# Performance work log

Measured on AMD Instinct MI355X. Metric: run time of the kernel, lower is better.

Reference implementation:

```python
import jax, jax.numpy as jnp
import numpy as np

N_NODES = 16384
N_EDGES = 65536
B = 256
L = 1000
BN_EPS = 1e-5


def _bn_last(h, g, b, m, v):
    # BatchNorm1d in eval mode over last (feature) axis
    return (h - m) / jnp.sqrt(v + BN_EPS) * g + b


def _bn_chan(h, g, b, m, v):
    # BatchNorm1d in eval mode over channel axis of [N, C, W]
    inv = g / jnp.sqrt(v + BN_EPS)
    return (h - m[None, :, None]) * inv[None, :, None] + b[None, :, None]


def _conv1d(x, W, b):
    # x: [N, C, W], W: [O, I, K], stride 1, VALID
    y = jax.lax.conv_general_dilated(x, W, (1,), 'VALID',
                                     dimension_numbers=('NCH', 'OIH', 'NCH'))
    return y + b[None, :, None]


def _forward(x, g1_W1, g1_b1, g1_W2, g1_b2, gW1, gb1, gW2, gb2,
             bn_gamma, bn_beta, bn_mean, bn_var, fcxd_W, fcxd_b, embed,
             c1_W, c1_b, c2_W, c2_b, c3_W, c3_b,
             cbn_gamma, cbn_beta, cbn_mean, cbn_var, fcxc_W, fcxc_b,
             bnfc_gamma, bnfc_beta, bnfc_mean, bnfc_var,
             fc1_W, fc1_b, fc2_W, fc2_b, out_W, out_b,
             edge_index, batch, target):
    src, dst = edge_index[0], edge_index[1]
    # GIN layer 1: out_i = MLP(x_i + sum_{j->i} x_j)  (eps = 0)
    agg = jax.ops.segment_sum(x[src], dst, num_segments=N_NODES)
    h = x + agg
    h = jnp.maximum(h @ g1_W1 + g1_b1, 0.0) @ g1_W2 + g1_b2
    h = _bn_last(jnp.maximum(h, 0.0), bn_gamma[0], bn_beta[0], bn_mean[0], bn_var[0])
    # GIN layers 2..5 (stacked params)
    for i in range(4):
        agg = jax.ops.segment_sum(h[src], dst, num_segments=N_NODES)
        t = h + agg
        t = jnp.maximum(t @ gW1[i] + gb1[i], 0.0) @ gW2[i] + gb2[i]
        h = _bn_last(jnp.maximum(t, 0.0), bn_gamma[i + 1], bn_beta[i + 1],
                     bn_mean[i + 1], bn_var[i + 1])
    # global_add_pool over graph ids
    pooled = jax.ops.segment_sum(h, batch, num_segments=B)          # [B, 32]
    xd = jnp.maximum(pooled @ fcxd_W + fcxd_b, 0.0)                 # [B, 128] (dropout: eval)
    # protein branch
    emb = embed[target]                                             # [B, L, 128]
    xd2 = jnp.broadcast_to(xd[:, None, :], (B, L, xd.shape[-1]))
    xc = jnp.concatenate([emb, xd2], axis=-1).transpose(0, 2, 1)    # [B, 256, L]
    conv_params = [(c1_W, c1_b), (c2_W, c2_b), (c3_W, c3_b)]
    for i in range(3):
        xc = _conv1d(xc, conv_params[i][0], conv_params[i][1])
        xc = jnp.maximum(_bn_chan(xc, cbn_gamma[i], cbn_beta[i],
                                  cbn_mean[i], cbn_var[i]), 0.0)
    xcm = jnp.max(xc, axis=-1)                                      # global max pool -> [B, 32]
    xcf = jnp.maximum(_bn_last(xcm @ fcxc_W + fcxc_b,
                               bnfc_gamma, bnfc_beta, bnfc_mean, bnfc_var), 0.0)
    z = jnp.concatenate([xd, xcf], axis=1)                          # [B, 256]
    z = jnp.maximum(z @ fc1_W + fc1_b, 0.0)
    z = jnp.maximum(z @ fc2_W + fc2_b, 0.0)
    return z @ out_W + out_b                                        # [B, 1]


def setup_inputs() -> dict:
    key = jax.random.key(0)
    ks = list(jax.random.split(key, 48))
    it = iter(range(48))
    f32 = jnp.float32

    def rn(sh, s=0.1):
        return jax.random.normal(ks[next(it)], sh, dtype=f32) * s

    def un(sh):
        return jax.random.uniform(ks[next(it)], sh, dtype=f32, minval=0.5, maxval=1.5)

    inp = {}
    inp['x'] = jax.random.normal(ks[next(it)], (N_NODES, 78), dtype=f32)
    inp['edge_index'] = jax.random.randint(ks[next(it)], (2, N_EDGES), 0, N_NODES, dtype=jnp.int32)
    inp['batch'] = jnp.sort(jax.random.randint(ks[next(it)], (N_NODES,), 0, B, dtype=jnp.int32))
    inp['target'] = jax.random.randint(ks[next(it)], (B, L), 0, 26, dtype=jnp.int32)
    inp['g1_W1'] = rn((78, 32)); inp['g1_b1'] = rn((32,))
    inp['g1_W2'] = rn((32, 32)); inp['g1_b2'] = rn((32,))
    inp['gW1'] = rn((4, 32, 32)); inp['gb1'] = rn((4, 32))
    inp['gW2'] = rn((4, 32, 32)); inp['gb2'] = rn((4, 32))
    inp['bn_gamma'] = un((5, 32)); inp['bn_beta'] = rn((5, 32))
    inp['bn_mean'] = rn((5, 32)); inp['bn_var'] = un((5, 32))
    inp['fcxd_W'] = rn((32, 128)); inp['fcxd_b'] = rn((128,))
    inp['embed'] = rn((26, 128), 1.0)
    inp['c1_W'] = rn((32, 256, 16)); inp['c1_b'] = rn((32,))
    inp['c2_W'] = rn((32, 32, 16)); inp['c2_b'] = rn((32,))
    inp['c3_W'] = rn((32, 32, 16)); inp['c3_b'] = rn((32,))
    inp['cbn_gamma'] = un((3, 32)); inp['cbn_beta'] = rn((3, 32))
    inp['cbn_mean'] = rn((3, 32)); inp['cbn_var'] = un((3, 32))
    inp['fcxc_W'] = rn((32, 128)); inp['fcxc_b'] = rn((128,))
    inp['bnfc_gamma'] = un((128,)); inp['bnfc_beta'] = rn((128,))
    inp['bnfc_mean'] = rn((128,)); inp['bnfc_var'] = un((128,))
    inp['fc1_W'] = rn((256, 1024)); inp['fc1_b'] = rn((1024,))
    inp['fc2_W'] = rn((1024, 256)); inp['fc2_b'] = rn((256,))
    inp['out_W'] = rn((256, 1)); inp['out_b'] = rn((1,))
    return inp


def reference(x, edge_index, batch, target, g1_W1, g1_b1, g1_W2, g1_b2,
              gW1, gb1, gW2, gb2, bn_gamma, bn_beta, bn_mean, bn_var,
              fcxd_W, fcxd_b, embed, c1_W, c1_b, c2_W, c2_b, c3_W, c3_b,
              cbn_gamma, cbn_beta, cbn_mean, cbn_var, fcxc_W, fcxc_b,
              bnfc_gamma, bnfc_beta, bnfc_mean, bnfc_var,
              fc1_W, fc1_b, fc2_W, fc2_b, out_W, out_b):
    return _forward(x, g1_W1, g1_b1, g1_W2, g1_b2, gW1, gb1, gW2, gb2,
                    bn_gamma, bn_beta, bn_mean, bn_var, fcxd_W, fcxd_b, embed,
                    c1_W, c1_b, c2_W, c2_b, c3_W, c3_b,
                    cbn_gamma, cbn_beta, cbn_mean, cbn_var, fcxc_W, fcxc_b,
                    bnfc_gamma, bnfc_beta, bnfc_mean, bnfc_var,
                    fc1_W, fc1_b, fc2_W, fc2_b, out_W, out_b,
                    edge_index, batch, target)
```

## Files before the change

### kernel.cpp

```cpp
#include <hip/hip_runtime.h>
#include <hip/hip_bf16.h>

typedef __hip_bfloat16 bf16;
__device__ __forceinline__ float b2f(bf16 v){ return __bfloat162float(v); }

typedef __attribute__((ext_vector_type(8))) short s8v;
typedef __attribute__((ext_vector_type(4))) float f4v;

#define N_NODES 16384
#define N_EDGES 65536
#define NB 256
#define LSEQ 1000
#define BN_EPS 1e-5f
#define W1O 985
#define W2O 970
#define W3O 955
#define C1S 988
#define C2S 976

__device__ int g_isf32;

__device__ __forceinline__ float LD(const void* p, int i, int f){
    return f ? ((const float*)p)[i] : b2f(((const bf16*)p)[i]);
}

__device__ __forceinline__ unsigned short f2b(float x){
    unsigned u = __float_as_uint(x);
    return (unsigned short)((u + 0x7FFFu + ((u >> 16) & 1u)) >> 16);
}
__device__ __forceinline__ float bb2f(unsigned short h){
    return __uint_as_float(((unsigned)h) << 16);
}

__global__ void k_dtype(const void* x){
    if (threadIdx.x != 0 || blockIdx.x != 0) return;
    const unsigned short* u = (const unsigned short*)x;
    int insane = 0;
    for (int i = 0; i < 512; i++){
        unsigned short h = u[i];
        int ex = (h >> 7) & 0xFF;
        if (!(h == 0 || (ex >= 96 && ex <= 142))) insane++;
    }
    g_isf32 = (insane > 50) ? 1 : 0;
}

__device__ float g_hA[N_NODES*32];
__device__ float g_hB[N_NODES*32];
__device__ float g_pooled[NB*32];
__device__ float g_xd[NB*128];
__device__ float g_P[16*26*32];
__device__ float g_wsum[32*128];
__device__ float g_xdb[NB*32];
__device__ float g_xcm[NB*32];
__device__ float g_xcf[NB*128];
__device__ float g_z1[NB*1024];
__device__ float g_z2[NB*256];
__device__ float g_c1o[NB*32*C1S];
__device__ float g_c2o[NB*32*C2S];
__device__ __attribute__((aligned(16))) unsigned short g_wf[2][32768];
__device__ int g_deg[N_NODES];
__device__ int g_cur[N_NODES];
__device__ int g_rowptr[N_NODES + 1];
__device__ int g_csrc[N_EDGES];
__device__ int g_gstart[NB + 1];

__global__ void k_zero(){
    int i = blockIdx.x*256 + threadIdx.x;
    if (i < N_NODES) g_deg[i] = 0;
    else g_xcm[i - N_NODES] = 0.f;
}

__global__ void k_count(const int* __restrict__ ei){
    int e = blockIdx.x*256 + threadIdx.x;
    atomicAdd(&g_deg[ei[N_EDGES + e]], 1);
}
__global__ __launch_bounds__(1024) void k_scan(){
    __shared__ int part[1024];
    int t = threadIdx.x;
    int base = t*16;
    int s = 0;
    #pragma unroll
    for (int i = 0; i < 16; i++) s += g_deg[base + i];
    part[t] = s;
    __syncthreads();
    for (int off = 1; off < 1024; off <<= 1){
        int v = (t >= off) ? part[t - off] : 0;
        __syncthreads();
        part[t] += v;
        __syncthreads();
    }
    int run = (t == 0) ? 0 : part[t - 1];
    for (int i = 0; i < 16; i++){
        g_rowptr[base + i] = run;
        g_cur[base + i] = run;
        run += g_deg[base + i];
    }
    if (t == 1023) g_rowptr[N_NODES] = run;
}
__global__ void k_fill(const int* __restrict__ ei){
    int e = blockIdx.x*256 + threadIdx.x;
    int d = ei[N_EDGES + e];
    int slot = atomicAdd(&g_cur[d], 1);
    g_csrc[slot] = ei[e];
}
__global__ void k_ranges(const int* __restrict__ batch){
    int b = threadIdx.x;
    int lo = 0, hi = N_NODES;
    while (lo < hi){ int mid = (lo + hi) >> 1; if (batch[mid] < b) lo = mid + 1; else hi = mid; }
    g_gstart[b] = lo;
    if (b == 0) g_gstart[NB] = N_NODES;
}

__global__ void k_wpack(const void* w2, const void* w3){
    const int F = g_isf32;
    int idx = blockIdx.x*256 + threadIdx.x;
    int sel = idx >> 15;
    int r = idx & 32767;
    int j = r & 7;
    int lane = (r >> 3) & 63;
    int hl = (r >> 9) & 1;
    int ogrp = (r >> 10) & 1;
    int ktg = r >> 11;
    int c = (lane >> 4)*8 + j;
    int o = ogrp*16 + (lane & 15);
    const void* Wt = sel ? w3 : w2;
    float wv = LD(Wt, o*512 + c*16 + ktg, F);
    unsigned short h = f2b(wv);
    g_wf[sel][r] = hl ? f2b(wv - bb2f(h)) : h;
}


__global__ __launch_bounds__(256) void k_proj78(const void* x, const void* W1)
{
    const int F = g_isf32;
    __shared__ float sW1[78*32];
    __shared__ float sx[8][78];
    int tid = threadIdx.x;
    for (int i = tid; i < 78*32; i += 256) sW1[i] = LD(W1, i, F);
    int nodeBase = blockIdx.x * 8;
    for (int i = tid; i < 8*78; i += 256){
        int ln = i / 78, f = i - ln*78;
        sx[ln][f] = LD(x, (nodeBase + ln)*78 + f, F);
    }
    __syncthreads();
    int ln = tid >> 5, j = tid & 31;
    float a = 0.f;
    #pragma unroll 6
    for (int i = 0; i < 78; i++) a += sx[ln][i] * sW1[i*32 + j];
    g_hA[(nodeBase + ln)*32 + j] = a;
}

__global__ __launch_bounds__(256) void k_gin1b(
    const void* b1, const void* W2, const void* b2,
    const void* bng, const void* bnb, const void* bnm, const void* bnv)
{
    const int F = g_isf32;
    __shared__ float sW2[32*32];
    __shared__ float sb1[32], sb2[32], sA[32], sB[32];
    __shared__ float st[8][32];
    int tid = threadIdx.x;
    for (int i = tid; i < 1024; i += 256) sW2[i] = LD(W2, i, F);
    if (tid < 32){
        sb1[tid] = LD(b1, tid, F); sb2[tid] = LD(b2, tid, F);
        float inv = LD(bng, tid, F) * rsqrtf(LD(bnv, tid, F) + BN_EPS);
        sA[tid] = inv;
        sB[tid] = LD(bnb, tid, F) - LD(bnm, tid, F) * inv;
    }
    __syncthreads();
    int ln = tid >> 5, j = tid & 31;
    int n = blockIdx.x*8 + ln;
    int rs = g_rowptr[n], re2 = g_rowptr[n + 1];
    float agg = 0.f;
    for (int e = rs; e < re2; e++) agg += g_hA[g_csrc[e]*32 + j];
    st[ln][j] = fmaxf(g_hA[n*32 + j] + agg + sb1[j], 0.f);
    __syncthreads();
    float t2 = sb2[j];
    #pragma unroll
    for (int i = 0; i < 32; i++) t2 += st[ln][i] * sW2[i*32 + j];
    t2 = fmaxf(t2, 0.f);
    g_hB[n*32 + j] = t2 * sA[j] + sB[j];
}

__global__ __launch_bounds__(256) void k_gin32L(
    const void* W1, const void* b1, const void* W2, const void* b2,
    const void* bng, const void* bnb, const void* bnm, const void* bnv, int l)
{
    const int F = g_isf32;
    const float* hin = (l & 1) ? g_hA : g_hB;
    float* hout = (l & 1) ? g_hB : g_hA;
    const int oW = l*1024, ob = l*32, obn = (l+1)*32;
    __shared__ float sW1[32*32], sW2[32*32];
    __shared__ float sb1[32], sb2[32], sA[32], sB[32];
    __shared__ float sh[8][32], st[8][32];
    int tid = threadIdx.x;
    for (int i = tid; i < 1024; i += 256){ sW1[i] = LD(W1, oW + i, F); sW2[i] = LD(W2, oW + i, F); }
    if (tid < 32){
        sb1[tid] = LD(b1, ob + tid, F); sb2[tid] = LD(b2, ob + tid, F);
        float inv = LD(bng, obn + tid, F) * rsqrtf(LD(bnv, obn + tid, F) + BN_EPS);
        sA[tid] = inv;
        sB[tid] = LD(bnb, obn + tid, F) - LD(bnm, obn + tid, F) * inv;
    }
    int ln = tid >> 5, j = tid & 31;
    int n = blockIdx.x*8 + ln;
    int rs = g_rowptr[n], re2 = g_rowptr[n + 1];
    float agg = 0.f;
    for (int e = rs; e < re2; e++) agg += hin[g_csrc[e]*32 + j];
    sh[ln][j] = hin[n*32 + j] + agg;
    __syncthreads();
    float t1 = sb1[j];
    #pragma unroll
    for (int i = 0; i < 32; i++) t1 += sh[ln][i] * sW1[i*32 + j];
    st[ln][j] = fmaxf(t1, 0.f);
    __syncthreads();
    float t2 = sb2[j];
    #pragma unroll
    for (int i = 0; i < 32; i++) t2 += st[ln][i] * sW2[i*32 + j];
    t2 = fmaxf(t2, 0.f);
    hout[n*32 + j] = t2 * sA[j] + sB[j];
}

__global__ __launch_bounds__(256) void k_pool(){
    __shared__ float red[8][32];
    int b = blockIdx.x, tid = threadIdx.x;
    int j = tid & 31, sub = tid >> 5;
    int s = g_gstart[b], e = g_gstart[b + 1];
    float a = 0.f;
    for (int n = s + sub; n < e; n += 8) a += g_hB[n*32 + j];
    red[sub][j] = a;
    __syncthreads();
    if (sub == 0){
        float r = red[0][j] + red[1][j] + red[2][j] + red[3][j]
                + red[4][j] + red[5][j] + red[6][j] + red[7][j];
        g_pooled[b*32 + j] = r;
    }
}

__global__ void k_xd(const void* W, const void* bias){
    const int F = g_isf32;
    __shared__ float sp[32];
    int b = blockIdx.x, j = threadIdx.x;
    if (j < 32) sp[j] = g_pooled[b*32 + j];
    __syncthreads();
    float a = LD(bias, j, F);
    #pragma unroll
    for (int i = 0; i < 32; i++) a += sp[i] * LD(W, i*128 + j, F);
    g_xd[b*128 + j] = fmaxf(a, 0.f);
}


__global__ void k_P(const void* embed, const void* c1W){
    const int F = g_isf32;
    int idx = blockIdx.x*256 + threadIdx.x;
    if (idx >= 16*26*32) return;
    int o = idx & 31;
    int t = (idx >> 5) % 26;
    int k = idx / (32*26);
    float a = 0.f;
    for (int c = 0; c < 128; c++)
        a += LD(embed, t*128 + c, F) * LD(c1W, o*4096 + c*16 + k, F);
    g_P[(k*26 + t)*32 + o] = a;
}

__global__ void k_wsum(const void* c1W){
    const int F = g_isf32;
    int idx = blockIdx.x*256 + threadIdx.x;
    int o = idx >> 7, c = idx & 127;
    float a = 0.f;
    #pragma unroll
    for (int k = 0; k < 16; k++) a += LD(c1W, o*4096 + (128 + c)*16 + k, F);
    g_wsum[o*128 + c] = a;
}

__global__ void k_xdbias(const void* c1b){
    const int F = g_isf32;
    int idx = blockIdx.x*256 + threadIdx.x;
    int b = idx >> 5, o = idx & 31;
    float a = LD(c1b, o, F);
    for (int c = 0; c < 128; c++) a += g_xd[b*128 + c] * g_wsum[o*128 + c];
    g_xdb[idx] = a;
}

__global__ __launch_bounds__(256) void k_conv1L(
    const int* __restrict__ target,
    const void* g, const void* be, const void* m, const void* v, int obn)
{
    const int F = g_isf32;
    __shared__ float sP[16*26*32];
    __shared__ int   stg[LSEQ];
    __shared__ float sxb[32], sA[32], sB[32];
    int b = blockIdx.x, tid = threadIdx.x;
    for (int i = tid; i < 16*26*32; i += 256) sP[i] = g_P[i];
    for (int i = tid; i < LSEQ; i += 256) stg[i] = target[b*LSEQ + i];
    if (tid < 32){
        sxb[tid] = g_xdb[b*32 + tid];
        float inv = LD(g, obn + tid, F) * rsqrtf(LD(v, obn + tid, F) + BN_EPS);
        sA[tid] = inv;
        sB[tid] = LD(be, obn + tid, F) - LD(m, obn + tid, F) * inv;
    }
    __syncthreads();
    int o = tid & 31, wsub = tid >> 5;
    float xb = sxb[o], aa = sA[o], bb = sB[o];
    for (int w = wsub; w < W1O; w += 8){
        float a = xb;
        #pragma unroll
        for (int k = 0; k < 16; k++)
            a += sP[(k*26 + stg[w + k])*32 + o];
        g_c1o[(b*32 + o)*C1S + w] = fmaxf(a * aa + bb, 0.f);
    }
}


#define CT_W 128
#define CT_R 144
#define CPAD 40

__global__ __launch_bounds__(256) void k_cmfma(
    int sel, int Wvalid, int Wout, int inStride,
    const void* bias, const void* g, const void* be,
    const void* m, const void* v, int obn)
{
    const int F = g_isf32;
    const float* in = (sel == 0) ? g_c1o : g_c2o;
    __shared__ __attribute__((aligned(16))) unsigned short sAh[CT_R*CPAD];
    __shared__ __attribute__((aligned(16))) unsigned short sAl[CT_R*CPAD];
    __shared__ float sSc[32], sOf[32];
    int tid = threadIdx.x;
    int b = blockIdx.x >> 3;
    int tile = blockIdx.x & 7;
    int wbase = tile * CT_W;

    for (int c = 0; c < 32; c++){
        const float* src = in + (b*32 + c)*inStride;
        if (tid < CT_R){
            int wg_ = wbase + tid;
            float xv = (wg_ < Wvalid) ? src[wg_] : 0.f;
            unsigned short h = f2b(xv);
            sAh[tid*CPAD + c] = h;
            sAl[tid*CPAD + c] = f2b(xv - bb2f(h));
        }
    }
    if (tid < 32){
        float inv = LD(g, obn + tid, F) * rsqrtf(LD(v, obn + tid, F) + BN_EPS);
        sSc[tid] = inv;
        sOf[tid] = LD(be, obn + tid, F) + (LD(bias, tid, F) - LD(m, obn + tid, F)) * inv;
    }
    __syncthreads();

    int lane = tid & 63;
    int wv = tid >> 6;
    int ml = lane & 15, quad = lane >> 4;
    int wgrp = wv & 1;
    int ogrp = wv >> 1;

    const s8v* wfb = (const s8v*)&g_wf[sel][0] + ogrp*128 + lane;

    f4v acc[4];
    #pragma unroll
    for (int mt = 0; mt < 4; mt++) acc[mt] = (f4v){0.f, 0.f, 0.f, 0.f};

    s8v nbh = wfb[0], nbl = wfb[64];
    for (int ktg = 0; ktg < 16; ktg++){
        s8v bh = nbh, bl = nbl;
        if (ktg < 15){
            nbh = wfb[(ktg + 1)*256];
            nbl = wfb[(ktg + 1)*256 + 64];
        }
        #pragma unroll
        for (int mt = 0; mt < 4; mt++){
            int row = wgrp*64 + mt*16 + ml + ktg;
            const int aidx = row*CPAD + quad*8;
            s8v ah = *(const s8v*)&sAh[aidx];
            s8v al = *(const s8v*)&sAl[aidx];
            acc[mt] = __builtin_amdgcn_mfma_f32_16x16x32_bf16(ah, bh, acc[mt], 0, 0, 0);
            acc[mt] = __builtin_amdgcn_mfma_f32_16x16x32_bf16(ah, bl, acc[mt], 0, 0, 0);
            acc[mt] = __builtin_amdgcn_mfma_f32_16x16x32_bf16(al, bh, acc[mt], 0, 0, 0);
        }
    }

    int o = ogrp*16 + ml;
    float sc = sSc[o], of = sOf[o];
    #pragma unroll
    for (int mt = 0; mt < 4; mt++){
        int w0 = wbase + wgrp*64 + mt*16 + quad*4;
        f4v a = acc[mt];
        float y0 = fmaxf(a.x*sc + of, 0.f);
        float y1 = fmaxf(a.y*sc + of, 0.f);
        float y2 = fmaxf(a.z*sc + of, 0.f);
        float y3 = fmaxf(a.w*sc + of, 0.f);
        if (sel == 0){
            float* dst = &g_c2o[(b*32 + o)*C2S + w0];
            if (w0 + 3 < Wout){
                *(float4*)dst = make_float4(y0, y1, y2, y3);
            } else if (w0 < Wout){
                dst[0] = y0;
                if (w0+1 < Wout) dst[1] = y1;
                if (w0+2 < Wout) dst[2] = y2;
                if (w0+3 < Wout) dst[3] = y3;
            }
        } else {
            if (w0 < Wout){
                float mx = y0;
                if (w0+1 < Wout) mx = fmaxf(mx, y1);
                if (w0+2 < Wout) mx = fmaxf(mx, y2);
                if (w0+3 < Wout) mx = fmaxf(mx, y3);
                atomicMax((int*)&g_xcm[b*32 + o], __float_as_int(mx));
            }
        }
    }
}


__global__ void k_xcf(const void* W, const void* bias,
                      const void* g, const void* be, const void* m, const void* v){
    const int F = g_isf32;
    __shared__ float sp[32];
    int b = blockIdx.x, j = threadIdx.x;
    if (j < 32) sp[j] = g_xcm[b*32 + j];
    __syncthreads();
    float a = LD(bias, j, F);
    #pragma unroll
    for (int i = 0; i < 32; i++) a += sp[i] * LD(W, i*128 + j, F);
    float inv = LD(g, j, F) * rsqrtf(LD(v, j, F) + BN_EPS);
    a = (a - LD(m, j, F)) * inv + LD(be, j, F);
    g_xcf[b*128 + j] = fmaxf(a, 0.f);
}

__global__ __launch_bounds__(256) void k_fc1(const void* W, const void* bias){
    const int F = g_isf32;
    __shared__ float sz[256];
    __shared__ float sp[2][128];
    int b = blockIdx.x >> 3;
    int jg = (blockIdx.x & 7) << 7;
    int t = threadIdx.x;
    sz[t] = (t < 128) ? g_xd[b*128 + t] : g_xcf[b*128 + (t - 128)];
    __syncthreads();
    int j = jg + (t & 127), half = t >> 7;
    float a = 0.f;
    #pragma unroll 8
    for (int i = half*128; i < half*128 + 128; i++)
        a += sz[i] * LD(W, i*1024 + j, F);
    sp[half][t & 127] = a;
    __syncthreads();
    if (t < 128){
        float r = sp[0][t] + sp[1][t] + LD(bias, jg + t, F);
        g_z1[b*1024 + jg + t] = fmaxf(r, 0.f);
    }
}

__global__ __launch_bounds__(1024) void k_fc2(const void* W, const void* bias){
    const int F = g_isf32;
    __shared__ float sz[1024];
    __shared__ float sp[4][256];
    int b = blockIdx.x, t = threadIdx.x;
    sz[t] = g_z1[b*1024 + t];
    __syncthreads();
    int j = t & 255, kq = t >> 8;
    float a = 0.f;
    #pragma unroll 8
    for (int i = 0; i < 256; i++)
        a += sz[kq*256 + i] * LD(W, (kq*256 + i)*256 + j, F);
    sp[kq][j] = a;
    __syncthreads();
    if (t < 256){
        float r = sp[0][t] + sp[1][t] + sp[2][t] + sp[3][t] + LD(bias, t, F);
        g_z2[b*256 + t] = fmaxf(r, 0.f);
    }
}

__global__ void k_out(const void* W, const void* bias, void* out){
    const int F = g_isf32;
    __shared__ float red[256];
    int b = blockIdx.x, t = threadIdx.x;
    red[t] = g_z2[b*256 + t] * LD(W, t, F);
    __syncthreads();
    for (int s = 128; s > 0; s >>= 1){
        if (t < s) red[t] += red[t + s];
        __syncthreads();
    }
    if (t == 0){
        float r = red[0] + LD(bias, 0, F);
        if (F) ((float*)out)[b] = r;
        else   ((bf16*)out)[b] = __float2bfloat16(r);
    }
}


extern "C" void kernel_launch(void* const* d_in, const int* in_sizes, int n_in,
                              void* d_out, int out_size, void* d_ws, size_t ws_size,
                              hipStream_t stream)
{
    (void)in_sizes; (void)n_in; (void)out_size; (void)d_ws; (void)ws_size;
    const void* x      = d_in[0];
    const int*  ei     = (const int*)d_in[1];
    const int*  batch  = (const int*)d_in[2];
    const int*  target = (const int*)d_in[3];
    const void* g1W1 = d_in[4];  const void* g1b1 = d_in[5];
    const void* g1W2 = d_in[6];  const void* g1b2 = d_in[7];
    const void* gW1  = d_in[8];  const void* gb1  = d_in[9];
    const void* gW2  = d_in[10]; const void* gb2  = d_in[11];
    const void* bng  = d_in[12]; const void* bnb  = d_in[13];
    const void* bnm  = d_in[14]; const void* bnv  = d_in[15];
    const void* fcxdW = d_in[16]; const void* fcxdb = d_in[17];
    const void* embed = d_in[18];
    const void* c1W = d_in[19]; const void* c1b = d_in[20];
    const void* c2W = d_in[21]; const void* c2b = d_in[22];
    const void* c3W = d_in[23]; const void* c3b = d_in[24];
    const void* cbng = d_in[25]; const void* cbnb = d_in[26];
    const void* cbnm = d_in[27]; const void* cbnv = d_in[28];
    const void* fcxcW = d_in[29]; const void* fcxcb = d_in[30];
    const void* bnfcg = d_in[31]; const void* bnfcb = d_in[32];
    const void* bnfcm = d_in[33]; const void* bnfcv = d_in[34];
    const void* fc1W = d_in[35]; const void* fc1b = d_in[36];
    const void* fc2W = d_in[37]; const void* fc2b = d_in[38];
    const void* outW = d_in[39]; const void* outb = d_in[40];

    k_dtype<<<1, 64, 0, stream>>>(x);
    k_wpack<<<256, 256, 0, stream>>>(c2W, c3W);

    k_zero<<<(N_NODES + NB*32)/256, 256, 0, stream>>>();
    k_count<<<N_EDGES/256, 256, 0, stream>>>(ei);
    k_scan<<<1, 1024, 0, stream>>>();
    k_fill<<<N_EDGES/256, 256, 0, stream>>>(ei);
    k_ranges<<<1, 256, 0, stream>>>(batch);

    k_proj78<<<N_NODES/8, 256, 0, stream>>>(x, g1W1);
    k_gin1b<<<N_NODES/8, 256, 0, stream>>>(g1b1, g1W2, g1b2, bng, bnb, bnm, bnv);
    for (int l = 0; l < 4; l++){
        k_gin32L<<<N_NODES/8, 256, 0, stream>>>(gW1, gb1, gW2, gb2,
                                                bng, bnb, bnm, bnv, l);
    }
    k_pool<<<NB, 256, 0, stream>>>();
    k_xd<<<NB, 128, 0, stream>>>(fcxdW, fcxdb);
    k_P<<<(16*26*32 + 255)/256, 256, 0, stream>>>(embed, c1W);
    k_wsum<<<16, 256, 0, stream>>>(c1W);
    k_xdbias<<<32, 256, 0, stream>>>(c1b);
    k_conv1L<<<NB, 256, 0, stream>>>(target, cbng, cbnb, cbnm, cbnv, 0);
    k_cmfma<<<NB*8, 256, 0, stream>>>(0, W1O, W2O, C1S,
                                      c2b, cbng, cbnb, cbnm, cbnv, 32);
    k_cmfma<<<NB*8, 256, 0, stream>>>(1, W2O, W3O, C2S,
                                      c3b, cbng, cbnb, cbnm, cbnv, 64);
    k_xcf<<<NB, 128, 0, stream>>>(fcxcW, fcxcb, bnfcg, bnfcb, bnfcm, bnfcv);
    k_fc1<<<NB*8, 256, 0, stream>>>(fc1W, fc1b);
    k_fc2<<<NB, 1024, 0, stream>>>(fc2W, fc2b);
    k_out<<<NB, 256, 0, stream>>>(outW, outb, d_out);
}
```

Measured before the change: 481.1 us.

## Fuse small tail kernels, split conv1 across blocks, warp-shuffle CSR gather

Merges pool with the xd projection, the P and wsum precompute kernels into one launch, and xcf, fc1, fc2 and out into a single per-sample tail kernel. Each conv1 sample is split across 4 blocks to raise parallelism. Neighbor indices in the CSR gather are now loaded cooperatively by the warp and broadcast with shuffles. This is meant to cut launch overhead and serialized index loads. The cost is that fc1 now runs with only 256 blocks, each reading all of fc1W, where it previously had 2048 blocks.

```diff
diff --git a/kernel.cpp b/kernel.cpp
--- a/kernel.cpp
+++ b/kernel.cpp
@@ -46,15 +46,11 @@
 
 __device__ float g_hA[N_NODES*32];
 __device__ float g_hB[N_NODES*32];
-__device__ float g_pooled[NB*32];
 __device__ float g_xd[NB*128];
 __device__ float g_P[16*26*32];
 __device__ float g_wsum[32*128];
 __device__ float g_xdb[NB*32];
 __device__ float g_xcm[NB*32];
-__device__ float g_xcf[NB*128];
-__device__ float g_z1[NB*1024];
-__device__ float g_z2[NB*256];
 __device__ float g_c1o[NB*32*C1S];
 __device__ float g_c2o[NB*32*C2S];
 __device__ __attribute__((aligned(16))) unsigned short g_wf[2][32768];
@@ -150,6 +146,21 @@
     g_hA[(nodeBase + ln)*32 + j] = a;
 }
 
+__device__ __forceinline__ float csr_gather(const float* hin, int n, int j){
+    int rs = g_rowptr[n];
+    int deg = g_rowptr[n + 1] - rs;
+    float agg = 0.f;
+    for (int base = 0; base < deg; base += 32){
+        int cnt = deg - base; if (cnt > 32) cnt = 32;
+        int myidx = (j < cnt) ? g_csrc[rs + base + j] : 0;
+        for (int e = 0; e < cnt; e++){
+            int src = __shfl(myidx, e, 32);
+            agg += hin[src*32 + j];
+        }
+    }
+    return agg;
+}
+
 __global__ __launch_bounds__(256) void k_gin1b(
     const void* b1, const void* W2, const void* b2,
     const void* bng, const void* bnb, const void* bnm, const void* bnv)
@@ -169,9 +180,7 @@
     __syncthreads();
     int ln = tid >> 5, j = tid & 31;
     int n = blockIdx.x*8 + ln;
-    int rs = g_rowptr[n], re2 = g_rowptr[n + 1];
-    float agg = 0.f;
-    for (int e = rs; e < re2; e++) agg += g_hA[g_csrc[e]*32 + j];
+    float agg = csr_gather(g_hA, n, j);
     st[ln][j] = fmaxf(g_hA[n*32 + j] + agg + sb1[j], 0.f);
     __syncthreads();
     float t2 = sb2[j];
@@ -202,9 +211,7 @@
     }
     int ln = tid >> 5, j = tid & 31;
     int n = blockIdx.x*8 + ln;
-    int rs = g_rowptr[n], re2 = g_rowptr[n + 1];
-    float agg = 0.f;
-    for (int e = rs; e < re2; e++) agg += hin[g_csrc[e]*32 + j];
+    float agg = csr_gather(hin, n, j);
     sh[ln][j] = hin[n*32 + j] + agg;
     __syncthreads();
     float t1 = sb1[j];
@@ -219,7 +226,8 @@
     hout[n*32 + j] = t2 * sA[j] + sB[j];
 }
 
-__global__ __launch_bounds__(256) void k_pool(){
+__global__ __launch_bounds__(256) void k_poolxd(const void* W, const void* bias){
+    const int F = g_isf32;
     __shared__ float red[8][32];
     int b = blockIdx.x, tid = threadIdx.x;
     int j = tid & 31, sub = tid >> 5;
@@ -229,46 +237,39 @@
     red[sub][j] = a;
     __syncthreads();
     if (sub == 0){
-        float r = red[0][j] + red[1][j] + red[2][j] + red[3][j]
-                + red[4][j] + red[5][j] + red[6][j] + red[7][j];
-        g_pooled[b*32 + j] = r;
-    }
-}
-
-__global__ void k_xd(const void* W, const void* bias){
-    const int F = g_isf32;
-    __shared__ float sp[32];
-    int b = blockIdx.x, j = threadIdx.x;
-    if (j < 32) sp[j] = g_pooled[b*32 + j];
-    __syncthreads();
-    float a = LD(bias, j, F);
-    #pragma unroll
-    for (int i = 0; i < 32; i++) a += sp[i] * LD(W, i*128 + j, F);
-    g_xd[b*128 + j] = fmaxf(a, 0.f);
-}
-
-
-__global__ void k_P(const void* embed, const void* c1W){
-    const int F = g_isf32;
-    int idx = blockIdx.x*256 + threadIdx.x;
-    if (idx >= 16*26*32) return;
-    int o = idx & 31;
-    int t = (idx >> 5) % 26;
-    int k = idx / (32*26);
-    float a = 0.f;
-    for (int c = 0; c < 128; c++)
-        a += LD(embed, t*128 + c, F) * LD(c1W, o*4096 + c*16 + k, F);
-    g_P[(k*26 + t)*32 + o] = a;
-}
-
-__global__ void k_wsum(const void* c1W){
-    const int F = g_isf32;
-    int idx = blockIdx.x*256 + threadIdx.x;
-    int o = idx >> 7, c = idx & 127;
-    float a = 0.f;
-    #pragma unroll
-    for (int k = 0; k < 16; k++) a += LD(c1W, o*4096 + (128 + c)*16 + k, F);
-    g_wsum[o*128 + c] = a;
+        red[0][j] = red[0][j] + red[1][j] + red[2][j] + red[3][j]
+                  + red[4][j] + red[5][j] + red[6][j] + red[7][j];
+    }
+    __syncthreads();
+    if (tid < 128){
+        float acc = LD(bias, tid, F);
+        #pragma unroll
+        for (int i = 0; i < 32; i++) acc += red[0][i] * LD(W, i*128 + tid, F);
+        g_xd[b*128 + tid] = fmaxf(acc, 0.f);
+    }
+}
+
+
+__global__ void k_Pw(const void* embed, const void* c1W){
+    const int F = g_isf32;
+    if (blockIdx.x < 52){
+        int idx = blockIdx.x*256 + threadIdx.x;
+        if (idx >= 16*26*32) return;
+        int o = idx & 31;
+        int t = (idx >> 5) % 26;
+        int k = idx / (32*26);
+        float a = 0.f;
+        for (int c = 0; c < 128; c++)
+            a += LD(embed, t*128 + c, F) * LD(c1W, o*4096 + c*16 + k, F);
+        g_P[(k*26 + t)*32 + o] = a;
+    } else {
+        int idx = (blockIdx.x - 52)*256 + threadIdx.x;
+        int o = idx >> 7, c = idx & 127;
+        float a = 0.f;
+        #pragma unroll
+        for (int k = 0; k < 16; k++) a += LD(c1W, o*4096 + (128 + c)*16 + k, F);
+        g_wsum[o*128 + c] = a;
+    }
 }
 
 __global__ void k_xdbias(const void* c1b){
@@ -288,7 +289,8 @@
     __shared__ float sP[16*26*32];
     __shared__ int   stg[LSEQ];
     __shared__ float sxb[32], sA[32], sB[32];
-    int b = blockIdx.x, tid = threadIdx.x;
+    int b = blockIdx.x >> 2, q = blockIdx.x & 3;
+    int tid = threadIdx.x;
     for (int i = tid; i < 16*26*32; i += 256) sP[i] = g_P[i];
     for (int i = tid; i < LSEQ; i += 256) stg[i] = target[b*LSEQ + i];
     if (tid < 32){
@@ -300,7 +302,9 @@
     __syncthreads();
     int o = tid & 31, wsub = tid >> 5;
     float xb = sxb[o], aa = sA[o], bb = sB[o];
-    for (int w = wsub; w < W1O; w += 8){
+    int wlo = q*248;
+    int whi = (q == 3) ? W1O : wlo + 248;
+    for (int w = wlo + wsub; w < whi; w += 8){
         float a = xb;
         #pragma unroll
         for (int k = 0; k < 16; k++)
@@ -410,75 +414,51 @@
 }
 
 
-__global__ void k_xcf(const void* W, const void* bias,
-                      const void* g, const void* be, const void* m, const void* v){
-    const int F = g_isf32;
-    __shared__ float sp[32];
-    int b = blockIdx.x, j = threadIdx.x;
-    if (j < 32) sp[j] = g_xcm[b*32 + j];
-    __syncthreads();
-    float a = LD(bias, j, F);
-    #pragma unroll
-    for (int i = 0; i < 32; i++) a += sp[i] * LD(W, i*128 + j, F);
-    float inv = LD(g, j, F) * rsqrtf(LD(v, j, F) + BN_EPS);
-    a = (a - LD(m, j, F)) * inv + LD(be, j, F);
-    g_xcf[b*128 + j] = fmaxf(a, 0.f);
-}
-
-__global__ __launch_bounds__(256) void k_fc1(const void* W, const void* bias){
+__global__ __launch_bounds__(1024) void k_tail(
+    const void* fcxcW, const void* fcxcb,
+    const void* bg, const void* bb, const void* bm, const void* bv,
+    const void* fc1W, const void* fc1b,
+    const void* fc2W, const void* fc2b,
+    const void* outW, const void* outb, void* out)
+{
     const int F = g_isf32;
     __shared__ float sz[256];
-    __shared__ float sp[2][128];
-    int b = blockIdx.x >> 3;
-    int jg = (blockIdx.x & 7) << 7;
-    int t = threadIdx.x;
-    sz[t] = (t < 128) ? g_xd[b*128 + t] : g_xcf[b*128 + (t - 128)];
-    __syncthreads();
-    int j = jg + (t & 127), half = t >> 7;
-    float a = 0.f;
-    #pragma unroll 8
-    for (int i = half*128; i < half*128 + 128; i++)
-        a += sz[i] * LD(W, i*1024 + j, F);
-    sp[half][t & 127] = a;
-    __syncthreads();
-    if (t < 128){
-        float r = sp[0][t] + sp[1][t] + LD(bias, jg + t, F);
-        g_z1[b*1024 + jg + t] = fmaxf(r, 0.f);
-    }
-}
-
-__global__ __launch_bounds__(1024) void k_fc2(const void* W, const void* bias){
-    const int F = g_isf32;
-    __shared__ float sz[1024];
+    __shared__ float z1s[1024];
     __shared__ float sp[4][256];
     int b = blockIdx.x, t = threadIdx.x;
-    sz[t] = g_z1[b*1024 + t];
+    if (t < 128) sz[t] = g_xd[b*128 + t];
+    else if (t < 256){
+        int j = t - 128;
+        float a = LD(fcxcb, j, F);
+        #pragma unroll
+        for (int i = 0; i < 32; i++) a += g_xcm[b*32 + i] * LD(fcxcW, i*128 + j, F);
+        float inv = LD(bg, j, F) * rsqrtf(LD(bv, j, F) + BN_EPS);
+        a = (a - LD(bm, j, F)) * inv + LD(bb, j, F);
+        sz[t] = fmaxf(a, 0.f);
+    }
+    __syncthreads();
+    float a = LD(fc1b, t, F);
+    for (int i = 0; i < 256; i++) a += sz[i] * LD(fc1W, i*1024 + t, F);
+    z1s[t] = fmaxf(a, 0.f);
     __syncthreads();
     int j = t & 255, kq = t >> 8;
-    float a = 0.f;
+    float a2 = 0.f;
     #pragma unroll 8
     for (int i = 0; i < 256; i++)
-        a += sz[kq*256 + i] * LD(W, (kq*256 + i)*256 + j, F);
-    sp[kq][j] = a;
+        a2 += z1s[kq*256 + i] * LD(fc2W, (kq*256 + i)*256 + j, F);
+    sp[kq][j] = a2;
     __syncthreads();
     if (t < 256){
-        float r = sp[0][t] + sp[1][t] + sp[2][t] + sp[3][t] + LD(bias, t, F);
-        g_z2[b*256 + t] = fmaxf(r, 0.f);
-    }
-}
-
-__global__ void k_out(const void* W, const void* bias, void* out){
-    const int F = g_isf32;
-    __shared__ float red[256];
-    int b = blockIdx.x, t = threadIdx.x;
-    red[t] = g_z2[b*256 + t] * LD(W, t, F);
+        float z2 = fmaxf(sp[0][t] + sp[1][t] + sp[2][t] + sp[3][t] + LD(fc2b, t, F), 0.f);
+        sp[0][t] = z2 * LD(outW, t, F);
+    }
     __syncthreads();
     for (int s = 128; s > 0; s >>= 1){
-        if (t < s) red[t] += red[t + s];
+        if (t < s) sp[0][t] += sp[0][t + s];
         __syncthreads();
     }
     if (t == 0){
-        float r = red[0] + LD(bias, 0, F);
+        float r = sp[0][0] + LD(outb, 0, F);
         if (F) ((float*)out)[b] = r;
         else   ((bf16*)out)[b] = __float2bfloat16(r);
     }
@@ -529,18 +509,14 @@
         k_gin32L<<<N_NODES/8, 256, 0, stream>>>(gW1, gb1, gW2, gb2,
                                                 bng, bnb, bnm, bnv, l);
     }
-    k_pool<<<NB, 256, 0, stream>>>();
-    k_xd<<<NB, 128, 0, stream>>>(fcxdW, fcxdb);
-    k_P<<<(16*26*32 + 255)/256, 256, 0, stream>>>(embed, c1W);
-    k_wsum<<<16, 256, 0, stream>>>(c1W);
+    k_poolxd<<<NB, 256, 0, stream>>>(fcxdW, fcxdb);
+    k_Pw<<<68, 256, 0, stream>>>(embed, c1W);
     k_xdbias<<<32, 256, 0, stream>>>(c1b);
-    k_conv1L<<<NB, 256, 0, stream>>>(target, cbng, cbnb, cbnm, cbnv, 0);
+    k_conv1L<<<NB*4, 256, 0, stream>>>(target, cbng, cbnb, cbnm, cbnv, 0);
     k_cmfma<<<NB*8, 256, 0, stream>>>(0, W1O, W2O, C1S,
                                       c2b, cbng, cbnb, cbnm, cbnv, 32);
     k_cmfma<<<NB*8, 256, 0, stream>>>(1, W2O, W3O, C2S,
                                       c3b, cbng, cbnb, cbnm, cbnv, 64);
-    k_xcf<<<NB, 128, 0, stream>>>(fcxcW, fcxcb, bnfcg, bnfcb, bnfcm, bnfcv);
-    k_fc1<<<NB*8, 256, 0, stream>>>(fc1W, fc1b);
-    k_fc2<<<NB, 1024, 0, stream>>>(fc2W, fc2b);
-    k_out<<<NB, 256, 0, stream>>>(outW, outb, d_out);
-}
+    k_tail<<<NB, 1024, 0, stream>>>(fcxcW, fcxcb, bnfcg, bnfcb, bnfcm, bnfcv,
+                                    fc1W, fc1b, fc2W, fc2b, outW, outb, d_out);
+}
```

New measurement: 481.4 us. About the same (+0.1%).
